# Performance work log

Measured on AMD Instinct MI355X. Metric: run time of the kernel, lower is better.

## Reference

```python
import jax, jax.numpy as jnp
import numpy as np

N = 50000      # nodes
E = 800000     # edges (avg degree 16)
DX = 28        # data.x features (num_node_features=32 minus forces_stack 3 + forces_norm 1)
F = 256        # conv channel dim = n_l3 + n_l4
EDIM = 26      # gaussian edge features: (5-0)/0.2 + 1
G = 64         # graphs in batch
STEP = 0.2


def _leaky(x):
    return jnp.where(x >= 0, x, 0.01 * x)  # torch LeakyReLU default slope


def setup_inputs() -> dict:
    key = jax.random.key(0)
    ks = jax.random.split(key, 32)

    def w(k, i, o):
        return (jax.random.normal(k, (i, o), jnp.float32) / np.sqrt(i)).astype(jnp.float32)

    inp = {
        "x": jax.random.normal(ks[0], (N, DX), jnp.float32),
        "forces_stack": jax.random.normal(ks[1], (N, 3), jnp.float32),
        "forces_norm": jax.random.uniform(ks[2], (N, 1), jnp.float32),
        "action_x": jax.random.normal(ks[3], (N, 3), jnp.float32),
        "edge_length": jax.random.uniform(ks[4], (E,), jnp.float32, 0.0, 5.0),
        # embedding MLP: 32 -> 256 -> 256 -> 128
        "emb_w1": w(ks[5], 32, 256), "emb_b1": jnp.zeros((256,), jnp.float32),
        "emb_w2": w(ks[6], 256, 256), "emb_b2": jnp.zeros((256,), jnp.float32),
        "emb_w3": w(ks[7], 256, 128), "emb_b3": jnp.zeros((128,), jnp.float32),
        # ln_act: 3 -> 128
        "act_w": w(ks[8], 3, 128), "act_b": jnp.zeros((128,), jnp.float32),
        # 3 CGConv layers, each with lin_f and lin_s: (2F+EDIM) -> F
        "conv_wf": jnp.stack([w(ks[9 + l], 2 * F + EDIM, F) for l in range(3)]),
        "conv_bf": jnp.zeros((3, F), jnp.float32),
        "conv_ws": jnp.stack([w(ks[12 + l], 2 * F + EDIM, F) for l in range(3)]),
        "conv_bs": jnp.zeros((3, F), jnp.float32),
        # desc head: 256 -> 256 -> 1
        "desc_w1": w(ks[15], F, 256), "desc_b1": jnp.zeros((256,), jnp.float32),
        "desc_w2": w(ks[16], 256, 1), "desc_b2": jnp.zeros((1,), jnp.float32),
        "edge_index": jax.random.randint(ks[17], (2, E), 0, N),
        "batch": jnp.sort(jax.random.randint(ks[18], (N,), 0, G)),
    }
    return inp


def reference(x, forces_stack, forces_norm, action_x, edge_length,
              emb_w1, emb_b1, emb_w2, emb_b2, emb_w3, emb_b3,
              act_w, act_b,
              conv_wf, conv_bf, conv_ws, conv_bs,
              desc_w1, desc_b1, desc_w2, desc_b2,
              edge_index, batch):
    # gaussian distance expansion: [E, 26]
    mus = jnp.arange(EDIM, dtype=jnp.float32) * STEP
    edge_attr = jnp.exp(-((edge_length[:, None] - mus) ** 2) / (STEP ** 2))

    # node embedding MLP
    h = jnp.concatenate([x, forces_stack, forces_norm], axis=1)  # [N, 32]
    h = _leaky(h @ emb_w1 + emb_b1)
    h = _leaky(h @ emb_w2 + emb_b2)
    h = _leaky(h @ emb_w3 + emb_b3)  # [N, 128]

    a = action_x @ act_w + act_b     # [N, 128]
    s = jnp.concatenate([h, a], axis=1)  # [N, 256]

    src, dst = edge_index[0], edge_index[1]  # messages flow src -> dst
    n = s.shape[0]
    for l in range(3):
        # CGConv (batch_norm=False, aggr='add'): z = [x_i, x_j, e_ij]
        z = jnp.concatenate([s[dst], s[src], edge_attr], axis=1)  # [E, 538]
        gate = jax.nn.sigmoid(z @ conv_wf[l] + conv_bf[l])
        core = jax.nn.softplus(z @ conv_ws[l] + conv_bs[l])
        agg = jax.ops.segment_sum(gate * core, dst, num_segments=n)
        s = s + agg  # residual inside CGConv
        if l < 2:
            s = _leaky(s)

    # global_add_pool over graphs, then desc MLP
    y = jax.ops.segment_sum(s, batch, num_segments=G)  # [G, 256]
    y = jax.nn.relu(y @ desc_w1 + desc_b1) @ desc_w2 + desc_b2  # [G, 1]
    return jnp.squeeze(y, -1)
```

## Files before the change

### kernel.cpp

```cpp
#include <hip/hip_runtime.h>
#include <hip/hip_bf16.h>

#define N_NODES 50000
#define NPAD    50048
#define N_EDGES 800000
#define EDIM 26
#define DXF 28
#define G_GRAPHS 64
#define NQ 2048

typedef __attribute__((ext_vector_type(8))) short short8v;
typedef __attribute__((ext_vector_type(4))) float f32x4;
typedef unsigned short u16;
typedef unsigned int u32;

__device__ __forceinline__ float leakyf(float x){ return x >= 0.f ? x : 0.01f*x; }
__device__ __forceinline__ u16 f2bf(float f){
  __hip_bfloat16 h = __float2bfloat16(f);
  return __builtin_bit_cast(u16, h);
}
__device__ __forceinline__ float bf2f(u16 u){
  return __builtin_bit_cast(float, (u32)u << 16);
}
__device__ __forceinline__ u32 packbf(float a, float b){
  return (u32)f2bf(a) | ((u32)f2bf(b) << 16);
}
__device__ __forceinline__ float lo16(u32 v){ return __builtin_bit_cast(float, v << 16); }
__device__ __forceinline__ float hi16(u32 v){ return __builtin_bit_cast(float, v & 0xffff0000u); }

__global__ __launch_bounds__(256) void prep_kernel(
    const float* __restrict__ cwf, const float* __restrict__ cws,
    const float* __restrict__ ew1, const float* __restrict__ ew2,
    const float* __restrict__ ew3,
    u16* __restrict__ Wpk, u16* __restrict__ w1pk,
    u16* __restrict__ w2pk, u16* __restrict__ w3pk)
{
  int tid = blockIdx.x*256 + threadIdx.x;
  u16 out[8];
  if (tid < 98304){
    int nn  = tid & 1023;
    int kb  = (tid >> 10) & 31;
    int lyr = tid >> 15;
    int side = nn >> 9, g = (nn >> 4) & 31, r = nn & 15;
    int type = g & 1, ch = (g >> 1)*16 + r;
    const float* W = (type ? cws : cwf) + (size_t)lyr*538*256;
    #pragma unroll
    for (int j=0;j<8;j++)
      out[j] = f2bf(W[(size_t)(side*256 + kb*8 + j)*256 + ch]);
    *reinterpret_cast<uint4*>(&Wpk[(size_t)tid*8]) = *reinterpret_cast<uint4*>(out);
  } else if (tid < 99328){
    int i = tid - 98304;  int kq = i >> 8, col = i & 255;
    #pragma unroll
    for (int j=0;j<8;j++) out[j] = f2bf(ew1[(kq*8+j)*256 + col]);
    *reinterpret_cast<uint4*>(&w1pk[(size_t)i*8]) = *reinterpret_cast<uint4*>(out);
  } else if (tid < 107520){
    int i = tid - 99328;  int kb = i >> 8, col = i & 255;
    #pragma unroll
    for (int j=0;j<8;j++) out[j] = f2bf(ew2[(kb*8+j)*256 + col]);
    *reinterpret_cast<uint4*>(&w2pk[(size_t)i*8]) = *reinterpret_cast<uint4*>(out);
  } else if (tid < 111616){
    int i = tid - 107520; int kb = i >> 7, col = i & 127;
    #pragma unroll
    for (int j=0;j<8;j++) out[j] = f2bf(ew3[(kb*8+j)*128 + col]);
    *reinterpret_cast<uint4*>(&w3pk[(size_t)i*8]) = *reinterpret_cast<uint4*>(out);
  }
}

__global__ __launch_bounds__(256) void tfs_kernel(
    const float* __restrict__ cwf, const float* __restrict__ cws,
    const float* __restrict__ cbf, const float* __restrict__ cbs,
    u32* __restrict__ TFS)
{
  int q = blockIdx.x & (NQ-1);
  int lyr = blockIdx.x >> 11;
  int c = threadIdx.x;
  const float* wf = cwf + (size_t)lyr*538*256 + (size_t)512*256;
  const float* ws = cws + (size_t)lyr*538*256 + (size_t)512*256;
  float f = cbf[lyr*256 + c], s = cbs[lyr*256 + c];
  float len = (float)q * (5.f/NQ);
  for (int k=0;k<EDIM;k++){
    float d = len - 0.2f*(float)k;
    float g = __expf(-25.f*d*d);
    f += g * wf[k*256 + c];
    s += g * ws[k*256 + c];
  }
  TFS[((size_t)lyr*NQ + q)*256 + c] = packbf(f, s);
}

__global__ __launch_bounds__(256) void embed_kernel(
    const float* __restrict__ x, const float* __restrict__ fs,
    const float* __restrict__ fn, const float* __restrict__ act,
    const u16* __restrict__ w1pk, const float* __restrict__ eb1,
    const u16* __restrict__ w2pk, const float* __restrict__ eb2,
    const u16* __restrict__ w3pk, const float* __restrict__ eb3,
    const float* __restrict__ aw,  const float* __restrict__ ab,
    u16* __restrict__ sB)
{
  __shared__ u16 inA[32*32];
  __shared__ float actS[32*4];
  __shared__ u16 h1[32*256];
  __shared__ u16 h2[32*256];
  const int t = threadIdx.x;
  const int w = t >> 6, l = t & 63, q = l >> 4, r16 = l & 15;
  const int node0 = blockIdx.x * 32;

  for (int idx=t; idx<1024; idx+=256){
    int n = idx >> 5, k = idx & 31;
    int node = node0 + n;
    float v = 0.f;
    if (node < N_NODES){
      if (k < DXF)      v = x[node*DXF + k];
      else if (k < 31)  v = fs[node*3 + (k - DXF)];
      else              v = fn[node];
    }
    inA[idx] = f2bf(v);
  }
  { int n = t >> 2, k = t & 3;
    float v = 0.f;
    if (n < 32 && k < 3 && node0 + n < N_NODES) v = act[(node0+n)*3 + k];
    if (n < 32) actS[t] = v; }
  __syncthreads();

  f32x4 acc[2][4];
  #pragma unroll
  for (int mi=0;mi<2;mi++)
    #pragma unroll
    for (int ni=0;ni<4;ni++){ acc[mi][ni][0]=0;acc[mi][ni][1]=0;acc[mi][ni][2]=0;acc[mi][ni][3]=0; }
  {
    short8v a[2], b[4];
    #pragma unroll
    for (int mi=0;mi<2;mi++)
      a[mi] = *reinterpret_cast<const short8v*>(&inA[(mi*16+r16)*32 + q*8]);
    #pragma unroll
    for (int ni=0;ni<4;ni++)
      b[ni] = *reinterpret_cast<const short8v*>(&w1pk[((size_t)q*256 + w*64 + ni*16 + r16)*8]);
    #pragma unroll
    for (int mi=0;mi<2;mi++)
      #pragma unroll
      for (int ni=0;ni<4;ni++)
        acc[mi][ni] = __builtin_amdgcn_mfma_f32_16x16x32_bf16(a[mi], b[ni], acc[mi][ni], 0,0,0);
  }
  #pragma unroll
  for (int ni=0;ni<4;ni++){
    int col = w*64 + ni*16 + r16;
    float bias = eb1[col];
    #pragma unroll
    for (int mi=0;mi<2;mi++)
      #pragma unroll
      for (int r=0;r<4;r++){
        int row = mi*16 + q*4 + r;
        h1[(row*256 + col) ^ ((row&7)<<3)] = f2bf(leakyf(acc[mi][ni][r] + bias));
      }
  }
  __syncthreads();

  #pragma unroll
  for (int mi=0;mi<2;mi++)
    #pragma unroll
    for (int ni=0;ni<4;ni++){ acc[mi][ni][0]=0;acc[mi][ni][1]=0;acc[mi][ni][2]=0;acc[mi][ni][3]=0; }
  for (int ks=0;ks<8;ks++){
    short8v a[2], b[4];
    #pragma unroll
    for (int mi=0;mi<2;mi++){
      int row = mi*16 + r16;
      a[mi] = *reinterpret_cast<const short8v*>(&h1[(row*256 + ks*32 + q*8) ^ ((row&7)<<3)]);
    }
    #pragma unroll
    for (int ni=0;ni<4;ni++)
      b[ni] = *reinterpret_cast<const short8v*>(&w2pk[((size_t)(ks*4+q)*256 + w*64 + ni*16 + r16)*8]);
    #pragma unroll
    for (int mi=0;mi<2;mi++)
      #pragma unroll
      for (int ni=0;ni<4;ni++)
        acc[mi][ni] = __builtin_amdgcn_mfma_f32_16x16x32_bf16(a[mi], b[ni], acc[mi][ni], 0,0,0);
  }
  #pragma unroll
  for (int ni=0;ni<4;ni++){
    int col = w*64 + ni*16 + r16;
    float bias = eb2[col];
    #pragma unroll
    for (int mi=0;mi<2;mi++)
      #pragma unroll
      for (int r=0;r<4;r++){
        int row = mi*16 + q*4 + r;
        h2[(row*256 + col) ^ ((row&7)<<3)] = f2bf(leakyf(acc[mi][ni][r] + bias));
      }
  }
  __syncthreads();

  if (w < 2){
    #pragma unroll
    for (int mi=0;mi<2;mi++)
      #pragma unroll
      for (int ni=0;ni<4;ni++){ acc[mi][ni][0]=0;acc[mi][ni][1]=0;acc[mi][ni][2]=0;acc[mi][ni][3]=0; }
    for (int ks=0;ks<8;ks++){
      short8v a[2], b[4];
      #pragma unroll
      for (int mi=0;mi<2;mi++){
        int row = mi*16 + r16;
        a[mi] = *reinterpret_cast<const short8v*>(&h2[(row*256 + ks*32 + q*8) ^ ((row&7)<<3)]);
      }
      #pragma unroll
      for (int ni=0;ni<4;ni++)
        b[ni] = *reinterpret_cast<const short8v*>(&w3pk[((size_t)(ks*4+q)*128 + w*64 + ni*16 + r16)*8]);
      #pragma unroll
      for (int mi=0;mi<2;mi++)
        #pragma unroll
        for (int ni=0;ni<4;ni++)
          acc[mi][ni] = __builtin_amdgcn_mfma_f32_16x16x32_bf16(a[mi], b[ni], acc[mi][ni], 0,0,0);
    }
    #pragma unroll
    for (int ni=0;ni<4;ni++){
      int col = w*64 + ni*16 + r16;
      float bias = eb3[col];
      #pragma unroll
      for (int mi=0;mi<2;mi++)
        #pragma unroll
        for (int r=0;r<4;r++){
          int row = mi*16 + q*4 + r;
          sB[(size_t)(node0+row)*256 + col] = f2bf(leakyf(acc[mi][ni][r] + bias));
        }
    }
  } else {
    int c = t - 128;
    float w0 = aw[c], w1 = aw[128+c], w2 = aw[256+c], bb = ab[c];
    for (int n=0;n<32;n++){
      float v = bb + actS[n*4]*w0 + actS[n*4+1]*w1 + actS[n*4+2]*w2;
      sB[(size_t)(node0+n)*256 + 128 + c] = f2bf(v);
    }
  }
}

__global__ void hist_kernel(const int* __restrict__ ei, int* __restrict__ cnt){
  int e = blockIdx.x*256 + threadIdx.x;
  if (e < N_EDGES) atomicAdd(&cnt[ei[N_EDGES + e]], 1);
}

__global__ __launch_bounds__(256) void scan1_kernel(
    const int* __restrict__ cnt, int* __restrict__ rowptr, int* __restrict__ partial){
  __shared__ int sd[256];
  int t = threadIdx.x; int idx = blockIdx.x*256 + t;
  int v = (idx < N_NODES) ? cnt[idx] : 0;
  sd[t] = v; __syncthreads();
  for (int off=1; off<256; off<<=1){
    int x2 = (t>=off) ? sd[t-off] : 0;
    __syncthreads();
    sd[t] += x2; __syncthreads();
  }
  if (idx < N_NODES) rowptr[idx] = sd[t] - v;
  if (t == 255) partial[blockIdx.x] = sd[255];
}

__global__ __launch_bounds__(256) void scan2_kernel(int* __restrict__ partial, int nb){
  __shared__ int sd[256];
  int t = threadIdx.x;
  int v = (t<nb) ? partial[t] : 0;
  sd[t] = v; __syncthreads();
  for (int off=1; off<256; off<<=1){
    int x2 = (t>=off) ? sd[t-off] : 0;
    __syncthreads();
    sd[t] += x2; __syncthreads();
  }
  if (t<nb) partial[t] = sd[t] - v;
}

__global__ __launch_bounds__(256) void scan3_kernel(
    int* __restrict__ rowptr, const int* __restrict__ partial, int* __restrict__ cursor){
  int idx = blockIdx.x*256 + threadIdx.x;
  if (idx < N_NODES){
    int v = rowptr[idx] + partial[blockIdx.x];
    rowptr[idx] = v; cursor[idx] = v;
  }
  if (idx == 0) rowptr[N_NODES] = N_EDGES;
}

__global__ __launch_bounds__(256) void scatter_kernel(
    const int* __restrict__ ei, const float* __restrict__ elen,
    int* __restrict__ cursor, u32* __restrict__ recP)
{
  int e = blockIdx.x*256 + threadIdx.x;
  if (e >= N_EDGES) return;
  int d = ei[N_EDGES + e];
  int pos = atomicAdd(&cursor[d], 1);
  int qq = (int)rintf(elen[e] * ((float)NQ/5.f));
  qq = min(max(qq,0), NQ-1);
  recP[pos] = (u32)ei[e] | ((u32)qq << 16);
}

__global__ __launch_bounds__(256) void proj_kernel(
    const u16* __restrict__ sB, const u16* __restrict__ Wl,
    u32* __restrict__ Pdst, u32* __restrict__ Psrc)
{
  const int t = threadIdx.x;
  const int w = t >> 6, l = t & 63, q = l >> 4, r16 = l & 15;
  const int m0 = blockIdx.x * 64;
  const int y  = blockIdx.y;

  f32x4 acc[4][8];
  #pragma unroll
  for (int mi=0;mi<4;mi++)
    #pragma unroll
    for (int ni=0;ni<8;ni++){ acc[mi][ni][0]=0;acc[mi][ni][1]=0;acc[mi][ni][2]=0;acc[mi][ni][3]=0; }

  for (int ks=0; ks<8; ks++){
    short8v a[4], b[8];
    #pragma unroll
    for (int mi=0;mi<4;mi++)
      a[mi] = *reinterpret_cast<const short8v*>(&sB[(size_t)(m0+mi*16+r16)*256 + ks*32 + q*8]);
    #pragma unroll
    for (int ni=0;ni<8;ni++)
      b[ni] = *reinterpret_cast<const short8v*>(&Wl[((size_t)(ks*4+q)*1024 + y*512 + w*128 + ni*16 + r16)*8]);
    #pragma unroll
    for (int mi=0;mi<4;mi++)
      #pragma unroll
      for (int ni=0;ni<8;ni++)
        acc[mi][ni] = __builtin_amdgcn_mfma_f32_16x16x32_bf16(a[mi], b[ni], acc[mi][ni], 0,0,0);
  }

  u32* outP = (y == 0) ? Pdst : Psrc;
  #pragma unroll
  for (int mi=0;mi<4;mi++){
    #pragma unroll
    for (int p=0;p<4;p++){
      int ch = w*64 + p*16 + r16;
      #pragma unroll
      for (int r=0;r<4;r++){
        int row = m0 + mi*16 + q*4 + r;
        outP[(size_t)row*256 + ch] = packbf(acc[mi][2*p][r], acc[mi][2*p+1][r]);
      }
    }
  }
}

__global__ __launch_bounds__(256) void csr_edge_kernel(
    const u32* __restrict__ Pdst, const u32* __restrict__ Psrc,
    u16* __restrict__ sB, const u32* __restrict__ TFSl,
    const int* __restrict__ rowptr, const u32* __restrict__ recP,
    int do_leaky)
{
  const int t = threadIdx.x;
  const int node = blockIdx.x;
  const int r0 = rowptr[node];
  const int deg = rowptr[node+1] - r0;

  u32 pd = Pdst[(size_t)node*256 + t];
  const float Pg0 = lo16(pd), Pc0 = hi16(pd);
  float accS = 0.f;

  u32 pv0=0, tv0=0, pv1=0, tv1=0;
  if (deg > 0){
    u32 r = recP[r0];
    pv0 = Psrc[(size_t)(r & 0xffffu)*256 + t];
    tv0 = TFSl[(size_t)(r >> 16)*256 + t];
  }
  if (deg > 1){
    u32 r = recP[r0+1];
    pv1 = Psrc[(size_t)(r & 0xffffu)*256 + t];
    tv1 = TFSl[(size_t)(r >> 16)*256 + t];
  }

  for (int i=0; i<deg; i++){
    u32 pv = pv0, tv = tv0;
    pv0 = pv1; tv0 = tv1;
    if (i+2 < deg){
      u32 r = recP[r0+i+2];
      pv1 = Psrc[(size_t)(r & 0xffffu)*256 + t];
      tv1 = TFSl[(size_t)(r >> 16)*256 + t];
    }
    float gf = Pg0 + lo16(pv) + lo16(tv);
    float gs = Pc0 + hi16(pv) + hi16(tv);
    float gate = 1.f/(1.f + __expf(-gf));
    float u = __expf(-fabsf(gs));
    float sp = fmaxf(gs, 0.f) + __logf(1.f + u);
    accS = fmaf(gate, sp, accS);
  }

  float v = bf2f(sB[(size_t)node*256 + t]) + accS;
  if (do_leaky) v = leakyf(v);
  sB[(size_t)node*256 + t] = f2bf(v);
}

__global__ __launch_bounds__(256) void pool_kernel(
    const u16* __restrict__ sB, const int* __restrict__ batch, float* __restrict__ y)
{
  const int t = threadIdx.x;
  int n0 = blockIdx.x * 64;
  int nend = min(n0 + 64, N_NODES);
  float acc = 0.f; int cur = -1;
  for (int n=n0; n<nend; n++){
    int g = batch[n];
    if (g != cur){
      if (cur >= 0) atomicAdd(&y[cur*256 + t], acc);
      acc = 0.f; cur = g;
    }
    acc += bf2f(sB[(size_t)n*256 + t]);
  }
  if (cur >= 0) atomicAdd(&y[cur*256 + t], acc);
}

__global__ __launch_bounds__(256) void desc_kernel(
    const float* __restrict__ y,
    const float* __restrict__ w1, const float* __restrict__ b1,
    const float* __restrict__ w2, const float* __restrict__ b2,
    float* __restrict__ out)
{
  __shared__ float yS[256];
  __shared__ float red[256];
  const int g = blockIdx.x, t = threadIdx.x;
  yS[t] = y[g*256 + t];
  __syncthreads();
  float acc = b1[t];
  for (int k4=0;k4<256;k4+=4){
    float4 v = *reinterpret_cast<const float4*>(&yS[k4]);
    acc += v.x*w1[(k4+0)*256+t] + v.y*w1[(k4+1)*256+t]
         + v.z*w1[(k4+2)*256+t] + v.w*w1[(k4+3)*256+t];
  }
  red[t] = fmaxf(acc, 0.f) * w2[t];
  __syncthreads();
  for (int off=128; off>0; off>>=1){
    if (t < off) red[t] += red[t+off];
    __syncthreads();
  }
  if (t == 0) out[g] = red[0] + b2[0];
}

extern "C" void kernel_launch(void* const* d_in, const int* in_sizes, int n_in,
                              void* d_out, int out_size, void* d_ws, size_t ws_size,
                              hipStream_t stream)
{
  const float* x    = (const float*)d_in[0];
  const float* fs   = (const float*)d_in[1];
  const float* fn   = (const float*)d_in[2];
  const float* act  = (const float*)d_in[3];
  const float* elen = (const float*)d_in[4];
  const float* ew1  = (const float*)d_in[5];
  const float* eb1  = (const float*)d_in[6];
  const float* ew2  = (const float*)d_in[7];
  const float* eb2  = (const float*)d_in[8];
  const float* ew3  = (const float*)d_in[9];
  const float* eb3  = (const float*)d_in[10];
  const float* aw   = (const float*)d_in[11];
  const float* ab   = (const float*)d_in[12];
  const float* cwf  = (const float*)d_in[13];
  const float* cbf  = (const float*)d_in[14];
  const float* cws  = (const float*)d_in[15];
  const float* cbs  = (const float*)d_in[16];
  const float* dw1  = (const float*)d_in[17];
  const float* db1  = (const float*)d_in[18];
  const float* dw2  = (const float*)d_in[19];
  const float* db2  = (const float*)d_in[20];
  const int*   ei   = (const int*)d_in[21];
  const int*   batch= (const int*)d_in[22];
  float* out = (float*)d_out;

  char* ws = (char*)d_ws;
  size_t off = 0;
  auto carve = [&](size_t bytes)->char*{
    char* p = ws + off; off += (bytes + 255) & ~(size_t)255; return p;
  };
  u16*  sB     = (u16*) carve((size_t)NPAD*256*2);
  u32*  Pdst   = (u32*) carve((size_t)NPAD*256*4);
  u32*  Psrc   = (u32*) carve((size_t)NPAD*256*4);
  u16*  Wpk    = (u16*) carve((size_t)3*32*1024*8*2);
  u16*  w1pk   = (u16*) carve((size_t)1024*8*2);
  u16*  w2pk   = (u16*) carve((size_t)8192*8*2);
  u16*  w3pk   = (u16*) carve((size_t)4096*8*2);
  u32*  TFS    = (u32*) carve((size_t)3*NQ*256*4);
  int*  rowptr = (int*) carve((size_t)(N_NODES+1)*4);
  int*  cursor = (int*) carve((size_t)N_NODES*4);
  int*  cnt    = (int*) carve((size_t)N_NODES*4);
  int*  partial= (int*) carve(256*4);
  u32*  recP   = (u32*) carve((size_t)N_EDGES*4);
  float* y     = (float*)carve((size_t)G_GRAPHS*256*4);
  if (off > ws_size) return;

  hipMemsetAsync(cnt, 0, (size_t)N_NODES*4, stream);
  hipMemsetAsync(y, 0, (size_t)G_GRAPHS*256*4, stream);

  prep_kernel<<<436, 256, 0, stream>>>(cwf, cws, ew1, ew2, ew3,
                                       Wpk, w1pk, w2pk, w3pk);
  tfs_kernel<<<3*NQ, 256, 0, stream>>>(cwf, cws, cbf, cbs, TFS);
  embed_kernel<<<NPAD/32, 256, 0, stream>>>(x, fs, fn, act,
      w1pk, eb1, w2pk, eb2, w3pk, eb3, aw, ab, sB);

  const int EB = (N_EDGES + 255)/256;
  const int SB = (N_NODES + 255)/256;
  hist_kernel<<<EB, 256, 0, stream>>>(ei, cnt);
  scan1_kernel<<<SB, 256, 0, stream>>>(cnt, rowptr, partial);
  scan2_kernel<<<1, 256, 0, stream>>>(partial, SB);
  scan3_kernel<<<SB, 256, 0, stream>>>(rowptr, partial, cursor);
  scatter_kernel<<<EB, 256, 0, stream>>>(ei, elen, cursor, recP);

  for (int l=0; l<3; l++){
    proj_kernel<<<dim3(NPAD/64, 2), 256, 0, stream>>>(
        sB, Wpk + (size_t)l*32*1024*8, Pdst, Psrc);
    csr_edge_kernel<<<N_NODES, 256, 0, stream>>>(
        Pdst, Psrc, sB, TFS + (size_t)l*NQ*256, rowptr, recP, (l<2) ? 1 : 0);
  }

  pool_kernel<<<(N_NODES+63)/64, 256, 0, stream>>>(sB, batch, y);
  desc_kernel<<<G_GRAPHS, 256, 0, stream>>>(y, dw1, db1, dw2, db2, out);
}
```

Measured before the change: 1.034 ms.

## Quantize gathered source projections to int8 with per-channel scales

Source-node projections that the edge kernel gathers per edge are now stored as packed int8 pairs instead of bf16 pairs, halving the bytes of that gather. A new pre-pass kernel recomputes part of the projection GEMM to find per-channel absolute maxima. It samples only 64 of every 256 rows and adds a fixed margin, with clamping for values outside the range. The edge kernel dequantizes with an FMA. This trades an extra partial GEMM launch and reduced numerical precision for lower gather bandwidth in the dominant edge loop.

After: 1.231 ms. 19.1% more time.

```diff
diff --git a/kernel.cpp b/kernel.cpp
--- a/kernel.cpp
+++ b/kernel.cpp
@@ -8,6 +8,7 @@
 #define DXF 28
 #define G_GRAPHS 64
 #define NQ 2048
+#define MARG 1.2f
 
 typedef __attribute__((ext_vector_type(8))) short short8v;
 typedef __attribute__((ext_vector_type(4))) float f32x4;
@@ -287,9 +288,66 @@
   recP[pos] = (u32)ei[e] | ((u32)qq << 16);
 }
 
-__global__ __launch_bounds__(256) void proj_kernel(
+__device__ __forceinline__ void proj_accum(
     const u16* __restrict__ sB, const u16* __restrict__ Wl,
-    u32* __restrict__ Pdst, u32* __restrict__ Psrc)
+    int m0, int y, int w, int q, int r16, f32x4 acc[4][8])
+{
+  #pragma unroll
+  for (int mi=0;mi<4;mi++)
+    #pragma unroll
+    for (int ni=0;ni<8;ni++){ acc[mi][ni][0]=0;acc[mi][ni][1]=0;acc[mi][ni][2]=0;acc[mi][ni][3]=0; }
+  for (int ks=0; ks<8; ks++){
+    short8v a[4], b[8];
+    #pragma unroll
+    for (int mi=0;mi<4;mi++)
+      a[mi] = *reinterpret_cast<const short8v*>(&sB[(size_t)(m0+mi*16+r16)*256 + ks*32 + q*8]);
+    #pragma unroll
+    for (int ni=0;ni<8;ni++)
+      b[ni] = *reinterpret_cast<const short8v*>(&Wl[((size_t)(ks*4+q)*1024 + y*512 + w*128 + ni*16 + r16)*8]);
+    #pragma unroll
+    for (int mi=0;mi<4;mi++)
+      #pragma unroll
+      for (int ni=0;ni<8;ni++)
+        acc[mi][ni] = __builtin_amdgcn_mfma_f32_16x16x32_bf16(a[mi], b[ni], acc[mi][ni], 0,0,0);
+  }
+}
+
+__global__ __launch_bounds__(256) void proj_scale_kernel(
+    const u16* __restrict__ sB, const u16* __restrict__ Wl,
+    u32* __restrict__ scaleU)
+{
+  __shared__ u32 smax[512];
+  const int t = threadIdx.x;
+  const int w = t >> 6, l = t & 63, q = l >> 4, r16 = l & 15;
+  const int m0 = blockIdx.x * 256;
+  for (int i=t;i<512;i+=256) smax[i] = 0;
+  __syncthreads();
+
+  f32x4 acc[4][8];
+  proj_accum(sB, Wl, m0, 1, w, q, r16, acc);
+
+  #pragma unroll
+  for (int p=0;p<4;p++){
+    int ch = w*64 + p*16 + r16;
+    float mf = 0.f, ms = 0.f;
+    #pragma unroll
+    for (int mi=0;mi<4;mi++)
+      #pragma unroll
+      for (int r=0;r<4;r++){
+        mf = fmaxf(mf, fabsf(acc[mi][2*p][r]));
+        ms = fmaxf(ms, fabsf(acc[mi][2*p+1][r]));
+      }
+    atomicMax(&smax[ch],       __float_as_uint(mf));
+    atomicMax(&smax[256 + ch], __float_as_uint(ms));
+  }
+  __syncthreads();
+  for (int i=t;i<512;i+=256) atomicMax(&scaleU[i], smax[i]);
+}
+
+__global__ __launch_bounds__(256) void proj_main_kernel(
+    const u16* __restrict__ sB, const u16* __restrict__ Wl,
+    u32* __restrict__ Pdst, u16* __restrict__ Psrc8,
+    const u32* __restrict__ scaleU)
 {
   const int t = threadIdx.x;
   const int w = t >> 6, l = t & 63, q = l >> 4, r16 = l & 15;
@@ -297,44 +355,47 @@
   const int y  = blockIdx.y;
 
   f32x4 acc[4][8];
-  #pragma unroll
-  for (int mi=0;mi<4;mi++)
-    #pragma unroll
-    for (int ni=0;ni<8;ni++){ acc[mi][ni][0]=0;acc[mi][ni][1]=0;acc[mi][ni][2]=0;acc[mi][ni][3]=0; }
-
-  for (int ks=0; ks<8; ks++){
-    short8v a[4], b[8];
-    #pragma unroll
-    for (int mi=0;mi<4;mi++)
-      a[mi] = *reinterpret_cast<const short8v*>(&sB[(size_t)(m0+mi*16+r16)*256 + ks*32 + q*8]);
-    #pragma unroll
-    for (int ni=0;ni<8;ni++)
-      b[ni] = *reinterpret_cast<const short8v*>(&Wl[((size_t)(ks*4+q)*1024 + y*512 + w*128 + ni*16 + r16)*8]);
-    #pragma unroll
-    for (int mi=0;mi<4;mi++)
-      #pragma unroll
-      for (int ni=0;ni<8;ni++)
-        acc[mi][ni] = __builtin_amdgcn_mfma_f32_16x16x32_bf16(a[mi], b[ni], acc[mi][ni], 0,0,0);
-  }
-
-  u32* outP = (y == 0) ? Pdst : Psrc;
-  #pragma unroll
-  for (int mi=0;mi<4;mi++){
+  proj_accum(sB, Wl, m0, y, w, q, r16, acc);
+
+  if (y == 0){
+    #pragma unroll
+    for (int mi=0;mi<4;mi++){
+      #pragma unroll
+      for (int p=0;p<4;p++){
+        int ch = w*64 + p*16 + r16;
+        #pragma unroll
+        for (int r=0;r<4;r++){
+          int row = m0 + mi*16 + q*4 + r;
+          Pdst[(size_t)row*256 + ch] = packbf(acc[mi][2*p][r], acc[mi][2*p+1][r]);
+        }
+      }
+    }
+  } else {
     #pragma unroll
     for (int p=0;p<4;p++){
       int ch = w*64 + p*16 + r16;
-      #pragma unroll
-      for (int r=0;r<4;r++){
-        int row = m0 + mi*16 + q*4 + r;
-        outP[(size_t)row*256 + ch] = packbf(acc[mi][2*p][r], acc[mi][2*p+1][r]);
-      }
+      float mf = __uint_as_float(scaleU[ch]);
+      float ms = __uint_as_float(scaleU[256 + ch]);
+      float invF = mf > 0.f ? 127.f/(MARG*mf) : 0.f;
+      float invS = ms > 0.f ? 127.f/(MARG*ms) : 0.f;
+      #pragma unroll
+      for (int mi=0;mi<4;mi++)
+        #pragma unroll
+        for (int r=0;r<4;r++){
+          int row = m0 + mi*16 + q*4 + r;
+          float qf = fminf(fmaxf(rintf(acc[mi][2*p][r]   * invF), -127.f), 127.f);
+          float qs = fminf(fmaxf(rintf(acc[mi][2*p+1][r] * invS), -127.f), 127.f);
+          int qfi = (int)qf, qsi = (int)qs;
+          Psrc8[(size_t)row*256 + ch] = (u16)((qfi & 0xff) | ((qsi & 0xff) << 8));
+        }
     }
   }
 }
 
 __global__ __launch_bounds__(256) void csr_edge_kernel(
-    const u32* __restrict__ Pdst, const u32* __restrict__ Psrc,
+    const u32* __restrict__ Pdst, const u16* __restrict__ Psrc8,
     u16* __restrict__ sB, const u32* __restrict__ TFSl,
+    const u32* __restrict__ scaleU,
     const int* __restrict__ rowptr, const u32* __restrict__ recP,
     int do_leaky)
 {
@@ -343,32 +404,37 @@
   const int r0 = rowptr[node];
   const int deg = rowptr[node+1] - r0;
 
+  const float sfc = __uint_as_float(scaleU[t])       * (MARG/127.f);
+  const float ssc = __uint_as_float(scaleU[256 + t]) * (MARG/127.f);
+
   u32 pd = Pdst[(size_t)node*256 + t];
   const float Pg0 = lo16(pd), Pc0 = hi16(pd);
   float accS = 0.f;
 
-  u32 pv0=0, tv0=0, pv1=0, tv1=0;
+  u16 pv0=0; u32 tv0=0; u16 pv1=0; u32 tv1=0;
   if (deg > 0){
     u32 r = recP[r0];
-    pv0 = Psrc[(size_t)(r & 0xffffu)*256 + t];
+    pv0 = Psrc8[(size_t)(r & 0xffffu)*256 + t];
     tv0 = TFSl[(size_t)(r >> 16)*256 + t];
   }
   if (deg > 1){
     u32 r = recP[r0+1];
-    pv1 = Psrc[(size_t)(r & 0xffffu)*256 + t];
+    pv1 = Psrc8[(size_t)(r & 0xffffu)*256 + t];
     tv1 = TFSl[(size_t)(r >> 16)*256 + t];
   }
 
   for (int i=0; i<deg; i++){
-    u32 pv = pv0, tv = tv0;
+    u16 pv = pv0; u32 tv = tv0;
     pv0 = pv1; tv0 = tv1;
     if (i+2 < deg){
       u32 r = recP[r0+i+2];
-      pv1 = Psrc[(size_t)(r & 0xffffu)*256 + t];
+      pv1 = Psrc8[(size_t)(r & 0xffffu)*256 + t];
       tv1 = TFSl[(size_t)(r >> 16)*256 + t];
     }
-    float gf = Pg0 + lo16(pv) + lo16(tv);
-    float gs = Pc0 + hi16(pv) + hi16(tv);
+    float fq = (float)(char)(pv & 0xff);
+    float sq = (float)(char)(pv >> 8);
+    float gf = fmaf(sfc, fq, Pg0 + lo16(tv));
+    float gs = fmaf(ssc, sq, Pc0 + hi16(tv));
     float gate = 1.f/(1.f + __expf(-gf));
     float u = __expf(-fabsf(gs));
     float sp = fmaxf(gs, 0.f) + __logf(1.f + u);
@@ -460,12 +526,13 @@
   };
   u16*  sB     = (u16*) carve((size_t)NPAD*256*2);
   u32*  Pdst   = (u32*) carve((size_t)NPAD*256*4);
-  u32*  Psrc   = (u32*) carve((size_t)NPAD*256*4);
+  u16*  Psrc8  = (u16*) carve((size_t)NPAD*256*2);
   u16*  Wpk    = (u16*) carve((size_t)3*32*1024*8*2);
   u16*  w1pk   = (u16*) carve((size_t)1024*8*2);
   u16*  w2pk   = (u16*) carve((size_t)8192*8*2);
   u16*  w3pk   = (u16*) carve((size_t)4096*8*2);
   u32*  TFS    = (u32*) carve((size_t)3*NQ*256*4);
+  u32*  scaleU = (u32*) carve((size_t)3*512*4);
   int*  rowptr = (int*) carve((size_t)(N_NODES+1)*4);
   int*  cursor = (int*) carve((size_t)N_NODES*4);
   int*  cnt    = (int*) carve((size_t)N_NODES*4);
@@ -475,6 +542,7 @@
   if (off > ws_size) return;
 
   hipMemsetAsync(cnt, 0, (size_t)N_NODES*4, stream);
+  hipMemsetAsync(scaleU, 0, (size_t)3*512*4, stream);
   hipMemsetAsync(y, 0, (size_t)G_GRAPHS*256*4, stream);
 
   prep_kernel<<<436, 256, 0, stream>>>(cwf, cws, ew1, ew2, ew3,
@@ -492,10 +560,14 @@
   scatter_kernel<<<EB, 256, 0, stream>>>(ei, elen, cursor, recP);
 
   for (int l=0; l<3; l++){
-    proj_kernel<<<dim3(NPAD/64, 2), 256, 0, stream>>>(
-        sB, Wpk + (size_t)l*32*1024*8, Pdst, Psrc);
+    const u16* Wl = Wpk + (size_t)l*32*1024*8;
+    u32* scaleL = scaleU + (size_t)l*512;
+    proj_scale_kernel<<<196, 256, 0, stream>>>(sB, Wl, scaleL);
+    proj_main_kernel<<<dim3(NPAD/64, 2), 256, 0, stream>>>(
+        sB, Wl, Pdst, Psrc8, scaleL);
     csr_edge_kernel<<<N_NODES, 256, 0, stream>>>(
-        Pdst, Psrc, sB, TFS + (size_t)l*NQ*256, rowptr, recP, (l<2) ? 1 : 0);
+        Pdst, Psrc8, sB, TFS + (size_t)l*NQ*256, scaleL,
+        rowptr, recP, (l<2) ? 1 : 0);
   }
 
   pool_kernel<<<(N_NODES+63)/64, 256, 0, stream>>>(sB, batch, y);
```
